# Performance work log

Hardware: AMD Instinct MI355X
Metric: run time of the kernel (lower is better)

## Reference

```python
import jax, jax.numpy as jnp
import numpy as np

NEG = -1000000000.0

def setup_inputs() -> dict:
    key = jax.random.key(0)
    k1, k2, k3, k4 = jax.random.split(key, 4)
    B, T, D, V = 64, 512, 768, 20
    embeddings = jax.random.normal(k1, (B, T, D), dtype=jnp.float32)
    embeddings_mask = jax.random.randint(k2, (B, T), 0, 2, dtype=jnp.int32)
    value_mask = jax.random.randint(k3, (B, V), 0, 2, dtype=jnp.int32)
    value_weight = jax.random.normal(k4, (V, D), dtype=jnp.float32)
    return {"embeddings": embeddings, "embeddings_mask": embeddings_mask,
            "value_mask": value_mask, "value_weight": value_weight}

def reference(embeddings, embeddings_mask, value_mask, value_weight):
    # value attention: scores[b,t,v] = <emb[b,t], W[v]>  (torch does bcast-mul-sum)
    emb_mask = embeddings_mask.astype(jnp.float32)          # (B,T)
    scores = jnp.einsum('btd,vd->btv', embeddings, value_weight)
    scores = scores * emb_mask[:, :, None]                   # mask tokens
    value_scores = scores.sum(axis=1)                        # (B,V)
    value_scores = value_scores + (1.0 - value_mask.astype(jnp.float32)) * NEG
    value_probs = jax.nn.softmax(value_scores, axis=-1)      # (B,V)
    value_embedding = jnp.einsum('bv,vd->bd', value_probs, value_weight)
    # attention pooling over tokens using value_embedding as query
    pooling_scores = jnp.einsum('btd,bd->bt', embeddings, value_embedding)
    pooling_scores = pooling_scores + (1.0 - emb_mask) * NEG
    pooling_probs = jax.nn.softmax(pooling_scores, axis=-1)  # (B,T)
    pooled_embedding = jnp.einsum('btd,bt->bd', embeddings, pooling_probs)
    return (value_embedding, pooled_embedding, value_probs, pooling_probs)
```

## Files before the change

kernel.cpp:

```cpp
#include <hip/hip_runtime.h>
#include <math.h>

#define B 64
#define T 512
#define D 768
#define D4 192
#define V 20
#define NEG -1000000000.0f
#define BPB 4
#define TPB 128
#define NW 16
#define NBLK (B * BPB)
#define MAGIC 0x5A17C3D9u

__device__ __forceinline__ void st_agent(float* p, float v) {
  __hip_atomic_store(p, v, __ATOMIC_RELAXED, __HIP_MEMORY_SCOPE_AGENT);
}
__device__ __forceinline__ float ld_agent(const float* p) {
  return __hip_atomic_load(p, __ATOMIC_RELAXED, __HIP_MEMORY_SCOPE_AGENT);
}
__device__ __forceinline__ void st_agent_u(unsigned* p, unsigned v) {
  __hip_atomic_store(p, v, __ATOMIC_RELAXED, __HIP_MEMORY_SCOPE_AGENT);
}
__device__ __forceinline__ unsigned ld_agent_u(const unsigned* p) {
  return __hip_atomic_load(p, __ATOMIC_RELAXED, __HIP_MEMORY_SCOPE_AGENT);
}

__global__ __launch_bounds__(1024, 4) void k_batch(
    const float4* __restrict__ emb4, const int* __restrict__ emask,
    const int* __restrict__ vmask, const float* __restrict__ W,
    float* __restrict__ vemb_out, float* __restrict__ pooled_out,
    float* __restrict__ vprobs_out, float* __restrict__ pprobs_out,
    float* __restrict__ ws) {
  const int bc = blockIdx.x, b = bc >> 2, q = bc & 3;
  const int tid = threadIdx.x, wave = tid >> 6, lane = tid & 63;

  float* pd = ws;
  float* accq = pd + B * BPB * V;
  float* mq = accq + B * BPB * D;
  float* lq = mq + B * BPB;
  unsigned* flagA = (unsigned*)(lq + B * BPB);
  unsigned* flagC = flagA + B * BPB;

  __shared__ float4 lacc[NW][D4];
  __shared__ float buf[D];
  __shared__ int sm[TPB], idx[TPB], scnt;
  __shared__ float ssc[TPB];
  __shared__ float sc[V], pr[V];
  __shared__ float lm[NW], ll[NW], co16[NW], co4q[BPB];
  __shared__ float sM, sinvL;

  if (tid < TPB) sm[tid] = emask[b * T + q * TPB + tid];
  __syncthreads();
  if (tid < 64) {
    unsigned long long b0 = __ballot(sm[tid] != 0);
    unsigned long long b1 = __ballot(sm[tid + 64] != 0);
    int n0 = (int)__popcll(b0);
    unsigned long long below = (1ull << tid) - 1ull;
    if (sm[tid]) idx[__popcll(b0 & below)] = tid;
    if (sm[tid + 64]) idx[n0 + __popcll(b1 & below)] = tid + 64;
    if (tid == 0) scnt = n0 + (int)__popcll(b1);
  }
  __syncthreads();
  const int cnt = scnt;
  const float4* eb = emb4 + ((size_t)b * T + (size_t)q * TPB) * D4;

  {
    float4 s0 = {0.f, 0.f, 0.f, 0.f}, s1 = s0, s2 = s0;
    int i = wave;
    for (; i + NW < cnt; i += 2 * NW) {
      const float4* pa = eb + (size_t)idx[i] * D4 + lane;
      const float4* pb = eb + (size_t)idx[i + NW] * D4 + lane;
      float4 a0 = pa[0], a1 = pa[64], a2 = pa[128];
      float4 b0 = pb[0], b1 = pb[64], b2 = pb[128];
      s0.x += a0.x + b0.x; s0.y += a0.y + b0.y;
      s0.z += a0.z + b0.z; s0.w += a0.w + b0.w;
      s1.x += a1.x + b1.x; s1.y += a1.y + b1.y;
      s1.z += a1.z + b1.z; s1.w += a1.w + b1.w;
      s2.x += a2.x + b2.x; s2.y += a2.y + b2.y;
      s2.z += a2.z + b2.z; s2.w += a2.w + b2.w;
    }
    if (i < cnt) {
      const float4* pa = eb + (size_t)idx[i] * D4 + lane;
      float4 a0 = pa[0], a1 = pa[64], a2 = pa[128];
      s0.x += a0.x; s0.y += a0.y; s0.z += a0.z; s0.w += a0.w;
      s1.x += a1.x; s1.y += a1.y; s1.z += a1.z; s1.w += a1.w;
      s2.x += a2.x; s2.y += a2.y; s2.z += a2.z; s2.w += a2.w;
    }
    lacc[wave][lane] = s0;
    lacc[wave][lane + 64] = s1;
    lacc[wave][lane + 128] = s2;
    __syncthreads();
    if (tid < D4) {
      float4 r = {0.f, 0.f, 0.f, 0.f};
      for (int w = 0; w < NW; ++w) {
        float4 a = lacc[w][tid];
        r.x += a.x; r.y += a.y; r.z += a.z; r.w += a.w;
      }
      *(float4*)&buf[4 * tid] = r;
    }
    __syncthreads();
    for (int v = wave; v < V; v += NW) {
      float p = 0.f;
      const float* wv = W + (size_t)v * D;
      for (int j = 0; j < 12; ++j) {
        int d = lane + 64 * j;
        p += buf[d] * wv[d];
      }
      for (int off = 32; off; off >>= 1) p += __shfl_xor(p, off, 64);
      if (lane == 0) st_agent(&pd[bc * V + v], p);
    }
  }

  __syncthreads();
  if (tid == 0) {
    st_agent_u(&flagA[bc], MAGIC);
    const unsigned* fa = &flagA[b * BPB];
    while (ld_agent_u(fa + 0) != MAGIC || ld_agent_u(fa + 1) != MAGIC ||
           ld_agent_u(fa + 2) != MAGIC || ld_agent_u(fa + 3) != MAGIC)
      __builtin_amdgcn_s_sleep(2);
  }
  __syncthreads();

  if (tid < V) {
    float s = 0.f;
    for (int qq = 0; qq < BPB; ++qq)
      s += ld_agent(&pd[(b * BPB + qq) * V + tid]);
    sc[tid] = s + (vmask[b * V + tid] ? 0.f : NEG);
  }
  __syncthreads();
  if (tid == 0) {
    float m = sc[0];
    for (int v = 1; v < V; ++v) m = fmaxf(m, sc[v]);
    float ssum = 0.f;
    for (int v = 0; v < V; ++v) {
      float e = __expf(sc[v] - m);
      pr[v] = e;
      ssum += e;
    }
    float inv = 1.f / ssum;
    for (int v = 0; v < V; ++v) {
      pr[v] *= inv;
      if (q == 0) vprobs_out[b * V + v] = pr[v];
    }
  }
  __syncthreads();
  if (tid < D) {
    float a = 0.f;
    for (int v = 0; v < V; ++v) a += pr[v] * W[(size_t)v * D + tid];
    buf[tid] = a;
    if (q == 0) vemb_out[(size_t)b * D + tid] = a;
  }
  __syncthreads();

  {
    const float4* vb = (const float4*)buf;
    float4 ve0 = vb[lane], ve1 = vb[lane + 64], ve2 = vb[lane + 128];
    float m = NEG, l = 0.f;
    float4 a0 = {0.f, 0.f, 0.f, 0.f}, a1 = a0, a2 = a0;
    int i = wave;
    for (; i + NW < cnt; i += 2 * NW) {
      int t0 = idx[i], t1 = idx[i + NW];
      const float4* qa = eb + (size_t)t0 * D4 + lane;
      const float4* qb = eb + (size_t)t1 * D4 + lane;
      float4 e0 = qa[0], e1 = qa[64], e2 = qa[128];
      float4 f0 = qb[0], f1 = qb[64], f2 = qb[128];
      float p0 = e0.x * ve0.x + e0.y * ve0.y + e0.z * ve0.z + e0.w * ve0.w +
                 e1.x * ve1.x + e1.y * ve1.y + e1.z * ve1.z + e1.w * ve1.w +
                 e2.x * ve2.x + e2.y * ve2.y + e2.z * ve2.z + e2.w * ve2.w;
      float p1 = f0.x * ve0.x + f0.y * ve0.y + f0.z * ve0.z + f0.w * ve0.w +
                 f1.x * ve1.x + f1.y * ve1.y + f1.z * ve1.z + f1.w * ve1.w +
                 f2.x * ve2.x + f2.y * ve2.y + f2.z * ve2.z + f2.w * ve2.w;
      for (int off = 32; off; off >>= 1) {
        p0 += __shfl_xor(p0, off, 64);
        p1 += __shfl_xor(p1, off, 64);
      }
      if (lane == 0) { ssc[t0] = p0; ssc[t1] = p1; }
      float mn = fmaxf(m, fmaxf(p0, p1));
      float scale = __expf(m - mn);
      float w0 = __expf(p0 - mn), w1 = __expf(p1 - mn);
      l = l * scale + w0 + w1;
      a0.x = a0.x * scale + w0 * e0.x + w1 * f0.x;
      a0.y = a0.y * scale + w0 * e0.y + w1 * f0.y;
      a0.z = a0.z * scale + w0 * e0.z + w1 * f0.z;
      a0.w = a0.w * scale + w0 * e0.w + w1 * f0.w;
      a1.x = a1.x * scale + w0 * e1.x + w1 * f1.x;
      a1.y = a1.y * scale + w0 * e1.y + w1 * f1.y;
      a1.z = a1.z * scale + w0 * e1.z + w1 * f1.z;
      a1.w = a1.w * scale + w0 * e1.w + w1 * f1.w;
      a2.x = a2.x * scale + w0 * e2.x + w1 * f2.x;
      a2.y = a2.y * scale + w0 * e2.y + w1 * f2.y;
      a2.z = a2.z * scale + w0 * e2.z + w1 * f2.z;
      a2.w = a2.w * scale + w0 * e2.w + w1 * f2.w;
      m = mn;
    }
    if (i < cnt) {
      int t0 = idx[i];
      const float4* qa = eb + (size_t)t0 * D4 + lane;
      float4 e0 = qa[0], e1 = qa[64], e2 = qa[128];
      float p0 = e0.x * ve0.x + e0.y * ve0.y + e0.z * ve0.z + e0.w * ve0.w +
                 e1.x * ve1.x + e1.y * ve1.y + e1.z * ve1.z + e1.w * ve1.w +
                 e2.x * ve2.x + e2.y * ve2.y + e2.z * ve2.z + e2.w * ve2.w;
      for (int off = 32; off; off >>= 1) p0 += __shfl_xor(p0, off, 64);
      if (lane == 0) ssc[t0] = p0;
      float mn = fmaxf(m, p0);
      float scale = __expf(m - mn);
      float w0 = __expf(p0 - mn);
      l = l * scale + w0;
      a0.x = a0.x * scale + w0 * e0.x; a0.y = a0.y * scale + w0 * e0.y;
      a0.z = a0.z * scale + w0 * e0.z; a0.w = a0.w * scale + w0 * e0.w;
      a1.x = a1.x * scale + w0 * e1.x; a1.y = a1.y * scale + w0 * e1.y;
      a1.z = a1.z * scale + w0 * e1.z; a1.w = a1.w * scale + w0 * e1.w;
      a2.x = a2.x * scale + w0 * e2.x; a2.y = a2.y * scale + w0 * e2.y;
      a2.z = a2.z * scale + w0 * e2.z; a2.w = a2.w * scale + w0 * e2.w;
      m = mn;
    }
    if (lane == 0) { lm[wave] = m; ll[wave] = l; }
    lacc[wave][lane] = a0;
    lacc[wave][lane + 64] = a1;
    lacc[wave][lane + 128] = a2;
    __syncthreads();
    if (tid == 0) {
      float M = NEG;
      for (int w = 0; w < NW; ++w) M = fmaxf(M, lm[w]);
      float L = 0.f;
      for (int w = 0; w < NW; ++w) {
        float cw = __expf(lm[w] - M);
        co16[w] = cw;
        L += ll[w] * cw;
      }
      st_agent(&mq[bc], M);
      st_agent(&lq[bc], L);
    }
    __syncthreads();
    if (tid < D4) {
      float4 r = {0.f, 0.f, 0.f, 0.f};
      for (int w = 0; w < NW; ++w) {
        float cw = co16[w];
        float4 a = lacc[w][tid];
        r.x += cw * a.x; r.y += cw * a.y;
        r.z += cw * a.z; r.w += cw * a.w;
      }
      float* pa = &accq[(size_t)bc * D + 4 * tid];
      st_agent(pa + 0, r.x);
      st_agent(pa + 1, r.y);
      st_agent(pa + 2, r.z);
      st_agent(pa + 3, r.w);
    }
  }

  __syncthreads();
  if (tid == 0) {
    st_agent_u(&flagC[bc], MAGIC);
    const unsigned* fcp = &flagC[b * BPB];
    while (ld_agent_u(fcp + 0) != MAGIC || ld_agent_u(fcp + 1) != MAGIC ||
           ld_agent_u(fcp + 2) != MAGIC || ld_agent_u(fcp + 3) != MAGIC)
      __builtin_amdgcn_s_sleep(2);
  }
  __syncthreads();

  if (tid == 0) {
    float mv[BPB], M = NEG;
    for (int qq = 0; qq < BPB; ++qq) {
      mv[qq] = ld_agent(&mq[b * BPB + qq]);
      M = fmaxf(M, mv[qq]);
    }
    float L = 0.f;
    for (int qq = 0; qq < BPB; ++qq)
      L += ld_agent(&lq[b * BPB + qq]) * __expf(mv[qq] - M);
    float invL = 1.f / L;
    for (int qq = 0; qq < BPB; ++qq) co4q[qq] = __expf(mv[qq] - M) * invL;
    sM = M;
    sinvL = invL;
  }
  __syncthreads();
  {
    const float M = sM, invL = sinvL;
    if (tid < D / BPB) {
      int d = q * (D / BPB) + tid;
      float r = 0.f;
      for (int qq = 0; qq < BPB; ++qq)
        r += co4q[qq] * ld_agent(&accq[(size_t)(b * BPB + qq) * D + d]);
      pooled_out[(size_t)b * D + d] = r;
    }
    if (tid < TPB) {
      pprobs_out[b * T + q * TPB + tid] =
          sm[tid] ? __expf(ssc[tid] - M) * invL : 0.f;
    }
  }
}

extern "C" void kernel_launch(void* const* d_in, const int* in_sizes, int n_in,
                              void* d_out, int out_size, void* d_ws,
                              size_t ws_size, hipStream_t stream) {
  const float4* emb4 = (const float4*)d_in[0];
  const int* emask = (const int*)d_in[1];
  const int* vmask = (const int*)d_in[2];
  const float* W = (const float*)d_in[3];

  float* out = (float*)d_out;
  float* vemb_out = out;
  float* pooled_out = out + B * D;
  float* vprobs_out = out + 2 * B * D;
  float* pprobs_out = out + 2 * B * D + B * V;

  float* ws = (float*)d_ws;

  k_batch<<<dim3(NBLK), dim3(1024), 0, stream>>>(emb4, emask, vmask, W,
                                                 vemb_out, pooled_out,
                                                 vprobs_out, pprobs_out, ws);
}
```

Before: 154.5 us.

## Split each batch across 8 smaller blocks and prefetch first pooling row before barrier

Each batch row is now split over 8 blocks of 512 threads (64 tokens each) instead of 4 blocks of 1024, so more smaller blocks are spread across the GPU. Each wave loads its first masked token row before the inter-block flag wait, so that load's latency overlaps the barrier spin. Partial accumulators are written and read as 8-byte atomic pairs. The cost is more inter-block partials to merge and a spin barrier that now waits on 8 co-resident blocks per batch, which depends on all of them being resident at once.

```diff
diff --git a/kernel.cpp b/kernel.cpp
--- a/kernel.cpp
+++ b/kernel.cpp
@@ -1,5 +1,6 @@
 #include <hip/hip_runtime.h>
 #include <math.h>
+#include <string.h>
 
 #define B 64
 #define T 512
@@ -7,9 +8,10 @@
 #define D4 192
 #define V 20
 #define NEG -1000000000.0f
-#define BPB 4
-#define TPB 128
-#define NW 16
+#define BPB 8
+#define TPB 64
+#define NW 8
+#define NTHR 512
 #define NBLK (B * BPB)
 #define MAGIC 0x5A17C3D9u
 
@@ -25,41 +27,50 @@
 __device__ __forceinline__ unsigned ld_agent_u(const unsigned* p) {
   return __hip_atomic_load(p, __ATOMIC_RELAXED, __HIP_MEMORY_SCOPE_AGENT);
 }
-
-__global__ __launch_bounds__(1024, 4) void k_batch(
+__device__ __forceinline__ void st_agent_f2(double* p, float x, float y) {
+  float2 f = {x, y};
+  double d;
+  memcpy(&d, &f, 8);
+  __hip_atomic_store(p, d, __ATOMIC_RELAXED, __HIP_MEMORY_SCOPE_AGENT);
+}
+__device__ __forceinline__ float2 ld_agent_f2(const double* p) {
+  double d = __hip_atomic_load(p, __ATOMIC_RELAXED, __HIP_MEMORY_SCOPE_AGENT);
+  float2 f;
+  memcpy(&f, &d, 8);
+  return f;
+}
+
+__global__ __launch_bounds__(NTHR, 4) void k_batch(
     const float4* __restrict__ emb4, const int* __restrict__ emask,
     const int* __restrict__ vmask, const float* __restrict__ W,
     float* __restrict__ vemb_out, float* __restrict__ pooled_out,
     float* __restrict__ vprobs_out, float* __restrict__ pprobs_out,
     float* __restrict__ ws) {
-  const int bc = blockIdx.x, b = bc >> 2, q = bc & 3;
+  const int bc = blockIdx.x, b = bc >> 3, q = bc & 7;
   const int tid = threadIdx.x, wave = tid >> 6, lane = tid & 63;
 
   float* pd = ws;
-  float* accq = pd + B * BPB * V;
-  float* mq = accq + B * BPB * D;
+  float* accq_f = pd + B * BPB * V;
+  float* mq = accq_f + B * BPB * D;
   float* lq = mq + B * BPB;
   unsigned* flagA = (unsigned*)(lq + B * BPB);
   unsigned* flagC = flagA + B * BPB;
+  double* accq2 = (double*)accq_f;
 
   __shared__ float4 lacc[NW][D4];
   __shared__ float buf[D];
   __shared__ int sm[TPB], idx[TPB], scnt;
   __shared__ float ssc[TPB];
   __shared__ float sc[V], pr[V];
-  __shared__ float lm[NW], ll[NW], co16[NW], co4q[BPB];
+  __shared__ float lm[NW], ll[NW], co8[NW], coq[BPB];
   __shared__ float sM, sinvL;
 
   if (tid < TPB) sm[tid] = emask[b * T + q * TPB + tid];
   __syncthreads();
   if (tid < 64) {
-    unsigned long long b0 = __ballot(sm[tid] != 0);
-    unsigned long long b1 = __ballot(sm[tid + 64] != 0);
-    int n0 = (int)__popcll(b0);
-    unsigned long long below = (1ull << tid) - 1ull;
-    if (sm[tid]) idx[__popcll(b0 & below)] = tid;
-    if (sm[tid + 64]) idx[n0 + __popcll(b1 & below)] = tid + 64;
-    if (tid == 0) scnt = n0 + (int)__popcll(b1);
+    unsigned long long bal = __ballot(sm[tid] != 0);
+    if (sm[tid]) idx[__popcll(bal & ((1ull << tid) - 1ull))] = tid;
+    if (tid == 0) scnt = (int)__popcll(bal);
   }
   __syncthreads();
   const int cnt = scnt;
@@ -112,13 +123,26 @@
     }
   }
 
+  const bool have0 = (wave < cnt);
+  int pt0 = 0;
+  float4 pe0 = {0, 0, 0, 0}, pe1 = pe0, pe2 = pe0;
+  if (have0) {
+    pt0 = idx[wave];
+    const float4* qa = eb + (size_t)pt0 * D4 + lane;
+    pe0 = qa[0]; pe1 = qa[64]; pe2 = qa[128];
+  }
+
   __syncthreads();
   if (tid == 0) {
     st_agent_u(&flagA[bc], MAGIC);
     const unsigned* fa = &flagA[b * BPB];
-    while (ld_agent_u(fa + 0) != MAGIC || ld_agent_u(fa + 1) != MAGIC ||
-           ld_agent_u(fa + 2) != MAGIC || ld_agent_u(fa + 3) != MAGIC)
+    for (;;) {
+      int ok = 1;
+      for (int qq = 0; qq < BPB; ++qq)
+        if (ld_agent_u(fa + qq) != MAGIC) { ok = 0; break; }
+      if (ok) break;
       __builtin_amdgcn_s_sleep(2);
+    }
   }
   __syncthreads();
 
@@ -145,11 +169,11 @@
     }
   }
   __syncthreads();
-  if (tid < D) {
+  for (int d = tid; d < D; d += NTHR) {
     float a = 0.f;
-    for (int v = 0; v < V; ++v) a += pr[v] * W[(size_t)v * D + tid];
-    buf[tid] = a;
-    if (q == 0) vemb_out[(size_t)b * D + tid] = a;
+    for (int v = 0; v < V; ++v) a += pr[v] * W[(size_t)v * D + d];
+    buf[d] = a;
+    if (q == 0) vemb_out[(size_t)b * D + d] = a;
   }
   __syncthreads();
 
@@ -158,7 +182,21 @@
     float4 ve0 = vb[lane], ve1 = vb[lane + 64], ve2 = vb[lane + 128];
     float m = NEG, l = 0.f;
     float4 a0 = {0.f, 0.f, 0.f, 0.f}, a1 = a0, a2 = a0;
-    int i = wave;
+    if (have0) {
+      float p0 = pe0.x * ve0.x + pe0.y * ve0.y + pe0.z * ve0.z +
+                 pe0.w * ve0.w + pe1.x * ve1.x + pe1.y * ve1.y +
+                 pe1.z * ve1.z + pe1.w * ve1.w + pe2.x * ve2.x +
+                 pe2.y * ve2.y + pe2.z * ve2.z + pe2.w * ve2.w;
+      for (int off = 32; off; off >>= 1) p0 += __shfl_xor(p0, off, 64);
+      if (lane == 0) ssc[pt0] = p0;
+      float w0 = 1.f;
+      m = p0;
+      l = w0;
+      a0.x = w0 * pe0.x; a0.y = w0 * pe0.y; a0.z = w0 * pe0.z; a0.w = w0 * pe0.w;
+      a1.x = w0 * pe1.x; a1.y = w0 * pe1.y; a1.z = w0 * pe1.z; a1.w = w0 * pe1.w;
+      a2.x = w0 * pe2.x; a2.y = w0 * pe2.y; a2.z = w0 * pe2.z; a2.w = w0 * pe2.w;
+    }
+    int i = wave + NW;
     for (; i + NW < cnt; i += 2 * NW) {
       int t0 = idx[i], t1 = idx[i + NW];
       const float4* qa = eb + (size_t)t0 * D4 + lane;
@@ -194,7 +232,7 @@
       a2.w = a2.w * scale + w0 * e2.w + w1 * f2.w;
       m = mn;
     }
-    if (i < cnt) {
+    for (; i < cnt; i += NW) {
       int t0 = idx[i];
       const float4* qa = eb + (size_t)t0 * D4 + lane;
       float4 e0 = qa[0], e1 = qa[64], e2 = qa[128];
@@ -226,7 +264,7 @@
       float L = 0.f;
       for (int w = 0; w < NW; ++w) {
         float cw = __expf(lm[w] - M);
-        co16[w] = cw;
+        co8[w] = cw;
         L += ll[w] * cw;
       }
       st_agent(&mq[bc], M);
@@ -236,26 +274,28 @@
     if (tid < D4) {
       float4 r = {0.f, 0.f, 0.f, 0.f};
       for (int w = 0; w < NW; ++w) {
-        float cw = co16[w];
+        float cw = co8[w];
         float4 a = lacc[w][tid];
         r.x += cw * a.x; r.y += cw * a.y;
         r.z += cw * a.z; r.w += cw * a.w;
       }
-      float* pa = &accq[(size_t)bc * D + 4 * tid];
-      st_agent(pa + 0, r.x);
-      st_agent(pa + 1, r.y);
-      st_agent(pa + 2, r.z);
-      st_agent(pa + 3, r.w);
+      double* pa = accq2 + (size_t)bc * (D / 2) + 2 * tid;
+      st_agent_f2(pa + 0, r.x, r.y);
+      st_agent_f2(pa + 1, r.z, r.w);
     }
   }
 
   __syncthreads();
   if (tid == 0) {
     st_agent_u(&flagC[bc], MAGIC);
-    const unsigned* fcp = &flagC[b * BPB];
-    while (ld_agent_u(fcp + 0) != MAGIC || ld_agent_u(fcp + 1) != MAGIC ||
-           ld_agent_u(fcp + 2) != MAGIC || ld_agent_u(fcp + 3) != MAGIC)
+    const unsigned* fc = &flagC[b * BPB];
+    for (;;) {
+      int ok = 1;
+      for (int qq = 0; qq < BPB; ++qq)
+        if (ld_agent_u(fc + qq) != MAGIC) { ok = 0; break; }
+      if (ok) break;
       __builtin_amdgcn_s_sleep(2);
+    }
   }
   __syncthreads();
 
@@ -269,19 +309,24 @@
     for (int qq = 0; qq < BPB; ++qq)
       L += ld_agent(&lq[b * BPB + qq]) * __expf(mv[qq] - M);
     float invL = 1.f / L;
-    for (int qq = 0; qq < BPB; ++qq) co4q[qq] = __expf(mv[qq] - M) * invL;
+    for (int qq = 0; qq < BPB; ++qq) coq[qq] = __expf(mv[qq] - M) * invL;
     sM = M;
     sinvL = invL;
   }
   __syncthreads();
   {
     const float M = sM, invL = sinvL;
-    if (tid < D / BPB) {
-      int d = q * (D / BPB) + tid;
-      float r = 0.f;
-      for (int qq = 0; qq < BPB; ++qq)
-        r += co4q[qq] * ld_agent(&accq[(size_t)(b * BPB + qq) * D + d]);
-      pooled_out[(size_t)b * D + d] = r;
+    if (tid < D / (2 * BPB)) {
+      float r0 = 0.f, r1 = 0.f;
+      for (int qq = 0; qq < BPB; ++qq) {
+        float2 f =
+            ld_agent_f2(accq2 + (size_t)(b * BPB + qq) * (D / 2) +
+                        q * (D / (2 * BPB)) + tid);
+        r0 += coq[qq] * f.x;
+        r1 += coq[qq] * f.y;
+      }
+      float2 r = {r0, r1};
+      *(float2*)&pooled_out[(size_t)b * D + q * (D / BPB) + 2 * tid] = r;
     }
     if (tid < TPB) {
       pprobs_out[b * T + q * TPB + tid] =
@@ -306,7 +351,7 @@
 
   float* ws = (float*)d_ws;
 
-  k_batch<<<dim3(NBLK), dim3(1024), 0, stream>>>(emb4, emask, vmask, W,
+  k_batch<<<dim3(NBLK), dim3(NTHR), 0, stream>>>(emb4, emask, vmask, W,
                                                  vemb_out, pooled_out,
                                                  vprobs_out, pprobs_out, ws);
 }
```

Result: slower. 158.8 us (+2.8%).
